# Optimization experiments

Hardware: AMD Instinct MI355X
Metric: run time of the kernel (lower is better)

The kernel has to match this reference:

```python
import jax, jax.numpy as jnp
import numpy as np

HIDDEN = 1024
N_HEADS = 16
N_KV = 4
HEAD_DIM = HIDDEN // N_HEADS  # 64


def setup_inputs() -> dict:
    key = jax.random.key(0)
    ks = jax.random.split(key, 10)
    B, S, D = 2, 2048, HIDDEN
    s = 0.02
    return {
        "hidden_states": jax.random.normal(ks[0], (B, S, D), jnp.float32),
        "attention_mask": jnp.ones((B, S), jnp.float32),
        "Wq": jax.random.normal(ks[1], (D, N_HEADS * HEAD_DIM), jnp.float32) * s,
        "bq": jnp.zeros((N_HEADS * HEAD_DIM,), jnp.float32),
        "Wk": jax.random.normal(ks[2], (D, N_KV * HEAD_DIM), jnp.float32) * s,
        "bk": jnp.zeros((N_KV * HEAD_DIM,), jnp.float32),
        "Wv": jax.random.normal(ks[3], (D, N_KV * HEAD_DIM), jnp.float32) * s,
        "bv": jnp.zeros((N_KV * HEAD_DIM,), jnp.float32),
        "Wo": jax.random.normal(ks[4], (D, D), jnp.float32) * s,
        "bo": jnp.zeros((D,), jnp.float32),
    }


def _rope(x):
    # x: [B, H, S, Dh]; half-split RoPE as in the torch module
    S, Dh = x.shape[-2], x.shape[-1]
    inv_freq = 1.0 / (10000.0 ** (jnp.arange(0, Dh, 2, dtype=jnp.float32) / Dh))
    freqs = jnp.arange(S, dtype=jnp.float32)[:, None] * inv_freq[None, :]  # [S, Dh/2]
    cos, sin = jnp.cos(freqs), jnp.sin(freqs)
    x1, x2 = jnp.split(x, 2, axis=-1)
    return jnp.concatenate([x1 * cos - x2 * sin, x1 * sin + x2 * cos], axis=-1)


def reference(hidden_states, attention_mask, Wq, bq, Wk, bk, Wv, bv, Wo, bo):
    B, S, D = hidden_states.shape
    q = (hidden_states @ Wq + bq).reshape(B, S, N_HEADS, HEAD_DIM).transpose(0, 2, 1, 3)
    k = (hidden_states @ Wk + bk).reshape(B, S, N_KV, HEAD_DIM).transpose(0, 2, 1, 3)
    v = (hidden_states @ Wv + bv).reshape(B, S, N_KV, HEAD_DIM).transpose(0, 2, 1, 3)
    q = _rope(q)
    k = _rope(k)
    rep = N_HEADS // N_KV
    k = jnp.repeat(k, rep, axis=1)  # [B, H, S, Dh]
    v = jnp.repeat(v, rep, axis=1)
    bias = (1.0 - attention_mask[:, None, None, :]) * -1e9  # [B,1,1,S]
    scores = jnp.einsum("bhqd,bhkd->bhqk", q, k) / jnp.sqrt(jnp.float32(HEAD_DIM))
    attn = jax.nn.softmax(scores + bias, axis=-1)
    out = jnp.einsum("bhqk,bhkd->bhqd", attn, v)
    out = out.transpose(0, 2, 1, 3).reshape(B, S, D)
    return out @ Wo + bo
```

## Files before the change

kernel.cpp:

```cpp
#include <hip/hip_runtime.h>

typedef __bf16 bf16;
typedef __attribute__((ext_vector_type(8))) __bf16 bf16x8;
typedef __attribute__((ext_vector_type(4))) __bf16 bf16x4;
typedef __attribute__((ext_vector_type(4))) float f32x4;

#define LOG2E 1.44269504088896340736f
#define QSCALE 0.18033688011112042f

__device__ inline void tr_tile(const float* __restrict__ in, bf16* __restrict__ out,
                               int R, int C, int bx, int by, int tid) {
    __shared__ float t[32][33];
    int tx = tid & 31, ty = tid >> 5;
    int rbase = by * 32, cbase = bx * 32;
#pragma unroll
    for (int i = 0; i < 4; i++) {
        int r = ty + i * 8;
        t[r][tx] = in[(size_t)(rbase + r) * C + cbase + tx];
    }
    __syncthreads();
#pragma unroll
    for (int i = 0; i < 4; i++) {
        int r = ty + i * 8;
        out[(size_t)(cbase + r) * R + rbase + tx] = (bf16)t[tx][r];
    }
}

__global__ __launch_bounds__(256) void prep_k(const float* __restrict__ X,
                                              const float* __restrict__ Wq,
                                              const float* __restrict__ Wk,
                                              const float* __restrict__ Wv,
                                              const float* __restrict__ Wo,
                                              const float* __restrict__ mask,
                                              bf16* __restrict__ Xb,
                                              bf16* __restrict__ WqT,
                                              bf16* __restrict__ WkT,
                                              bf16* __restrict__ WvT,
                                              bf16* __restrict__ WoT,
                                              float2* __restrict__ rt,
                                              float* __restrict__ Mb,
                                              int* __restrict__ mflags) {
    int blk = blockIdx.x, tid = threadIdx.x;
    if (blk < 2048) {
        int idx = (blk * 256 + tid) * 8;
        float4 a = *(const float4*)(X + idx);
        float4 b = *(const float4*)(X + idx + 4);
        bf16 v[8] = {(bf16)a.x, (bf16)a.y, (bf16)a.z, (bf16)a.w,
                     (bf16)b.x, (bf16)b.y, (bf16)b.z, (bf16)b.w};
        *(uint4*)(Xb + idx) = *(const uint4*)v;
    } else if (blk < 3072) {
        int t = blk - 2048; tr_tile(Wq, WqT, 1024, 1024, t & 31, t >> 5, tid);
    } else if (blk < 3328) {
        int t = blk - 3072; tr_tile(Wk, WkT, 1024, 256, t & 7, t >> 3, tid);
    } else if (blk < 3584) {
        int t = blk - 3328; tr_tile(Wv, WvT, 1024, 256, t & 7, t >> 3, tid);
    } else if (blk < 4608) {
        int t = blk - 3584; tr_tile(Wo, WoT, 1024, 1024, t & 31, t >> 5, tid);
    } else if (blk < 4864) {
        int idx = (blk - 4608) * 256 + tid;
        int s = idx >> 5, i = idx & 31;
        float inv = exp2f(-0.41524100370589830f * (float)i);
        float ang = (float)s * inv;
        rt[idx] = make_float2(cosf(ang), sinf(ang));
    } else {
        __shared__ int sflag;
        int b = blk - 4864;
        if (tid == 0) sflag = 1;
        __syncthreads();
        const float* mrow = mask + (size_t)b * 2048;
        int i0 = tid * 8;
        bool ones = true;
#pragma unroll
        for (int j = 0; j < 8; j++) {
            float m = mrow[i0 + j];
            if (m != 1.0f) ones = false;
            Mb[(size_t)b * 2048 + i0 + j] = (1.0f - m) * (-1e9f) * LOG2E;
        }
        if (!ones) sflag = 0;
        __syncthreads();
        if (tid == 0) mflags[b] = sflag;
    }
}

__global__ __launch_bounds__(256) void vtrans_k(const unsigned short* __restrict__ in,
                                                unsigned short* __restrict__ out) {
    __shared__ unsigned short t[32][33];
    int z = blockIdx.z;
    const unsigned short* ip = in + (size_t)z * 2048 * 64;
    unsigned short* op = out + (size_t)z * 2048 * 64;
    int tx = threadIdx.x & 31, ty = threadIdx.x >> 5;
    int rbase = blockIdx.y * 32, cbase = blockIdx.x * 32;
#pragma unroll
    for (int i = 0; i < 4; i++) {
        int r = ty + i * 8;
        t[r][tx] = ip[(size_t)(rbase + r) * 64 + cbase + tx];
    }
    __syncthreads();
#pragma unroll
    for (int i = 0; i < 4; i++) {
        int r = ty + i * 8;
        op[(size_t)(cbase + r) * 2048 + rbase + tx] = t[tx][r];
    }
}

__device__ __forceinline__ void gemm_main_12864(const bf16* __restrict__ A,
                                                const bf16* __restrict__ BT,
                                                int m0, int n0, int tid,
                                                f32x4 (&acc)[2][4]) {
    __shared__ bf16 As[128 * 64];
    __shared__ bf16 Bs[64 * 64];
    int w = tid >> 6, lane = tid & 63, l15 = lane & 15, quad = lane >> 4;

    int srow = lane >> 3;
    int kx = ((lane & 7) ^ srow) * 8;
    const bf16* ga0 = A + (size_t)(m0 + w * 32 + srow) * 1024 + kx;
    const bf16* gb0 = BT + (size_t)(n0 + w * 16 + srow) * 1024 + kx;
    bf16* la0 = As + (w * 32) * 64 + lane * 8;
    bf16* lb0 = Bs + (w * 16) * 64 + lane * 8;

    for (int k0 = 0; k0 < 1024; k0 += 64) {
#pragma unroll
        for (int p = 0; p < 4; p++)
            __builtin_amdgcn_global_load_lds(
                (const __attribute__((address_space(1))) unsigned int*)(ga0 + (size_t)p * 8 * 1024 + k0),
                (__attribute__((address_space(3))) unsigned int*)(la0 + p * 512), 16, 0, 0);
#pragma unroll
        for (int p = 0; p < 2; p++)
            __builtin_amdgcn_global_load_lds(
                (const __attribute__((address_space(1))) unsigned int*)(gb0 + (size_t)p * 8 * 1024 + k0),
                (__attribute__((address_space(3))) unsigned int*)(lb0 + p * 512), 16, 0, 0);
        __syncthreads();
#pragma unroll
        for (int half = 0; half < 2; half++) {
            bf16x8 a[2], bfr[4];
            int kp = ((half * 4 + quad) ^ (l15 & 7)) * 8;
#pragma unroll
            for (int i = 0; i < 2; i++)
                a[i] = *(const bf16x8*)&As[(w * 32 + i * 16 + l15) * 64 + kp];
#pragma unroll
            for (int j = 0; j < 4; j++)
                bfr[j] = *(const bf16x8*)&Bs[(j * 16 + l15) * 64 + kp];
#pragma unroll
            for (int i = 0; i < 2; i++)
#pragma unroll
                for (int j = 0; j < 4; j++)
                    acc[i][j] = __builtin_amdgcn_mfma_f32_16x16x32_bf16(a[i], bfr[j], acc[i][j], 0, 0, 0);
        }
        __syncthreads();
    }
}

__global__ __launch_bounds__(256) void qkv_gemm2(const bf16* __restrict__ Xb,
                                                 const bf16* __restrict__ WTall,
                                                 const float* __restrict__ bq,
                                                 const float* __restrict__ bk,
                                                 const float* __restrict__ bv,
                                                 const float2* __restrict__ rt,
                                                 bf16* __restrict__ Qb,
                                                 bf16* __restrict__ Kb,
                                                 bf16* __restrict__ Vb) {
    int tt = blockIdx.x, gy = blockIdx.y, tid = threadIdx.x;
    f32x4 acc[2][4] = {};
    gemm_main_12864(Xb, WTall, tt * 128, gy * 64, tid, acc);

    int w = tid >> 6, lane = tid & 63, l15 = lane & 15, quad = lane >> 4;
    const float* bias;
    bf16* dst;
    int mode, head;
    if (gy < 16)      { head = gy;      bias = bq + head * 64; dst = Qb; mode = 0; }
    else if (gy < 20) { head = gy - 16; bias = bk + head * 64; dst = Kb; mode = 1; }
    else              { head = gy - 20; bias = bv + head * 64; dst = Vb; mode = 2; }

#pragma unroll
    for (int i = 0; i < 2; i++) {
#pragma unroll
        for (int r = 0; r < 4; r++) {
            int token = tt * 128 + w * 32 + i * 16 + quad * 4 + r;
            int b = token >> 11, s = token & 2047;
            float vals[4];
#pragma unroll
            for (int j = 0; j < 4; j++) vals[j] = acc[i][j][r] + bias[j * 16 + l15];
            if (mode <= 1) {
#pragma unroll
                for (int c = 0; c < 2; c++) {
                    float2 cs2 = rt[s * 32 + c * 16 + l15];
                    float x1 = vals[c], x2 = vals[c + 2];
                    vals[c]     = x1 * cs2.x - x2 * cs2.y;
                    vals[c + 2] = x1 * cs2.y + x2 * cs2.x;
                }
            }
            if (mode == 0) {
#pragma unroll
                for (int j = 0; j < 4; j++) vals[j] *= QSCALE;
            }
            size_t base;
            if (mode == 0) base = (((size_t)b * 16 + head) * 2048 + s) * 64;
            else           base = (((size_t)b * 4  + head) * 2048 + s) * 64;
#pragma unroll
            for (int j = 0; j < 4; j++) dst[base + j * 16 + l15] = (bf16)vals[j];
        }
    }
}

__global__ __launch_bounds__(256) void oproj_gemm2(const bf16* __restrict__ Ab,
                                                   const bf16* __restrict__ WoT,
                                                   const float* __restrict__ bo,
                                                   float* __restrict__ out) {
    int tt = blockIdx.x, nt = blockIdx.y, tid = threadIdx.x;
    f32x4 acc[2][4] = {};
    gemm_main_12864(Ab, WoT, tt * 128, nt * 64, tid, acc);

    int w = tid >> 6, lane = tid & 63, l15 = lane & 15, quad = lane >> 4;
#pragma unroll
    for (int i = 0; i < 2; i++) {
#pragma unroll
        for (int r = 0; r < 4; r++) {
            int token = tt * 128 + w * 32 + i * 16 + quad * 4 + r;
#pragma unroll
            for (int j = 0; j < 4; j++) {
                int n = nt * 64 + j * 16 + l15;
                out[(size_t)token * 1024 + n] = acc[i][j][r] + bo[n];
            }
        }
    }
}

__global__ __launch_bounds__(256) void attn_k(const bf16* __restrict__ Qb,
                                              const bf16* __restrict__ Kb,
                                              const bf16* __restrict__ VbT,
                                              const float* __restrict__ Mb,
                                              const int* __restrict__ mflags,
                                              bf16* __restrict__ Ob) {
    int qt = blockIdx.x, h = blockIdx.y, b = blockIdx.z;
    int kvh = h >> 2;

    __shared__ bf16 Ks[2][64 * 64];
    __shared__ bf16 Vs[2][64 * 64];
    __shared__ unsigned short Ps[4][32 * 72];

    int tid = threadIdx.x, w = tid >> 6, lane = tid & 63, l15 = lane & 15, quad = lane >> 4;

    const bool maskOnes = (mflags[b] != 0);

    bf16x8 qa[2][2];
#pragma unroll
    for (int g = 0; g < 2; g++) {
        size_t qbase = (((size_t)b * 16 + h) * 2048 + (size_t)qt * 128 + w * 32 + g * 16 + l15) * 64;
        qa[g][0] = *(const bf16x8*)(Qb + qbase + quad * 8);
        qa[g][1] = *(const bf16x8*)(Qb + qbase + 32 + quad * 8);
    }

    f32x4 oacc[2][4] = {};
    float lsum[2] = {0.f, 0.f};

    size_t kRow = ((size_t)b * 4 + kvh) * 2048;
    size_t vRow = ((size_t)b * 4 + kvh) * 64;
    const float* mrow = Mb + (size_t)b * 2048 + quad * 4;

    int srow = (lane >> 3);
    int kx = ((lane & 7) ^ srow) * 8;
    const bf16* gk0 = Kb + (kRow + w * 16 + srow) * 64 + kx;
    const bf16* gv0 = VbT + (vRow + w * 16 + srow) * 2048 + kx;
    int lofs = (w * 16) * 64 + lane * 8;

#define STAGE(KT, BUF)                                                                              \
    do {                                                                                            \
        _Pragma("unroll")                                                                           \
        for (int p = 0; p < 2; p++) {                                                               \
            __builtin_amdgcn_global_load_lds(                                                       \
                (const __attribute__((address_space(1))) unsigned int*)(gk0 + ((size_t)(KT) * 64 + p * 8) * 64), \
                (__attribute__((address_space(3))) unsigned int*)(&Ks[BUF][0] + lofs + p * 512), 16, 0, 0); \
            __builtin_amdgcn_global_load_lds(                                                       \
                (const __attribute__((address_space(1))) unsigned int*)(gv0 + (size_t)p * 8 * 2048 + (KT) * 64), \
                (__attribute__((address_space(3))) unsigned int*)(&Vs[BUF][0] + lofs + p * 512), 16, 0, 0); \
        }                                                                                           \
    } while (0)

    STAGE(0, 0);
    __syncthreads();

    for (int kt = 0; kt < 32; kt++) {
        int cb = kt & 1;
        if (kt < 31) STAGE(kt + 1, cb ^ 1);

        const bf16* ksb = &Ks[cb][0];
        const bf16* vsb = &Vs[cb][0];

        bf16x8 ka[4][2];
#pragma unroll
        for (int c = 0; c < 4; c++) {
            int row = c * 16 + l15;
#pragma unroll
            for (int half = 0; half < 2; half++) {
                int kp = ((half * 4 + quad) ^ (l15 & 7)) * 8;
                ka[c][half] = *(const bf16x8*)&ksb[row * 64 + kp];
            }
        }

        f32x4 sc[2][4];
#pragma unroll
        for (int g = 0; g < 2; g++)
#pragma unroll
            for (int c = 0; c < 4; c++) {
                f32x4 z = {};
                z = __builtin_amdgcn_mfma_f32_16x16x32_bf16(ka[c][0], qa[g][0], z, 0, 0, 0);
                z = __builtin_amdgcn_mfma_f32_16x16x32_bf16(ka[c][1], qa[g][1], z, 0, 0, 0);
                sc[g][c] = z;
            }
        if (!maskOnes) {
#pragma unroll
            for (int c = 0; c < 4; c++) {
                f32x4 bias4 = *(const f32x4*)(mrow + kt * 64 + c * 16);
#pragma unroll
                for (int r = 0; r < 4; r++) { sc[0][c][r] += bias4[r]; sc[1][c][r] += bias4[r]; }
            }
        }

#pragma unroll
        for (int g = 0; g < 2; g++) {
            float rs = 0.f;
#pragma unroll
            for (int c = 0; c < 4; c++)
#pragma unroll
                for (int r = 0; r < 4; r++) { sc[g][c][r] = exp2f(sc[g][c][r]); rs += sc[g][c][r]; }
            lsum[g] += rs;
#pragma unroll
            for (int c = 0; c < 4; c++) {
                bf16x4 pv = {(bf16)sc[g][c][0], (bf16)sc[g][c][1], (bf16)sc[g][c][2], (bf16)sc[g][c][3]};
                *(bf16x4*)&Ps[w][(g * 16 + l15) * 72 + c * 16 + quad * 4] = pv;
            }
        }

        bf16x8 vb[4][2];
#pragma unroll
        for (int c = 0; c < 4; c++) {
            int row = c * 16 + l15;
#pragma unroll
            for (int half = 0; half < 2; half++) {
                int kp = ((half * 4 + quad) ^ (l15 & 7)) * 8;
                vb[c][half] = *(const bf16x8*)&vsb[row * 64 + kp];
            }
        }
        bf16x8 pa[2][2];
#pragma unroll
        for (int g = 0; g < 2; g++) {
            pa[g][0] = *(const bf16x8*)&Ps[w][(g * 16 + l15) * 72 + quad * 8];
            pa[g][1] = *(const bf16x8*)&Ps[w][(g * 16 + l15) * 72 + 32 + quad * 8];
        }
#pragma unroll
        for (int g = 0; g < 2; g++)
#pragma unroll
            for (int c = 0; c < 4; c++) {
                oacc[g][c] = __builtin_amdgcn_mfma_f32_16x16x32_bf16(pa[g][0], vb[c][0], oacc[g][c], 0, 0, 0);
                oacc[g][c] = __builtin_amdgcn_mfma_f32_16x16x32_bf16(pa[g][1], vb[c][1], oacc[g][c], 0, 0, 0);
            }
        __syncthreads();
    }
#undef STAGE

#pragma unroll
    for (int g = 0; g < 2; g++) {
        lsum[g] += __shfl_xor(lsum[g], 16, 64);
        lsum[g] += __shfl_xor(lsum[g], 32, 64);
        float linv[4];
#pragma unroll
        for (int r = 0; r < 4; r++) linv[r] = 1.0f / __shfl(lsum[g], quad * 4 + r, 64);
#pragma unroll
        for (int r = 0; r < 4; r++) {
            int q = qt * 128 + w * 32 + g * 16 + quad * 4 + r;
            size_t base = ((size_t)b * 2048 + q) * 1024 + h * 64;
#pragma unroll
            for (int c = 0; c < 4; c++) Ob[base + c * 16 + l15] = (bf16)(oacc[g][c][r] * linv[r]);
        }
    }
}

extern "C" void kernel_launch(void* const* d_in, const int* in_sizes, int n_in,
                              void* d_out, int out_size, void* d_ws, size_t ws_size,
                              hipStream_t stream) {
    const float* X    = (const float*)d_in[0];
    const float* mask = (const float*)d_in[1];
    const float* Wq   = (const float*)d_in[2];
    const float* bq   = (const float*)d_in[3];
    const float* Wk   = (const float*)d_in[4];
    const float* bk   = (const float*)d_in[5];
    const float* Wv   = (const float*)d_in[6];
    const float* bv   = (const float*)d_in[7];
    const float* Wo   = (const float*)d_in[8];
    const float* bo   = (const float*)d_in[9];
    float* out = (float*)d_out;
    bf16* ws  = (bf16*)d_ws;

    bf16* Xb  = ws;
    bf16* WqT = Xb + (size_t)4096 * 1024;
    bf16* WkT = WqT + 1024 * 1024;
    bf16* WvT = WkT + 256 * 1024;
    bf16* WoT = WvT + 256 * 1024;
    bf16* Qb  = WoT + 1024 * 1024;
    bf16* Kb  = Qb + (size_t)2 * 16 * 2048 * 64;
    bf16* Vb  = Kb + (size_t)2 * 4 * 2048 * 64;
    bf16* Ab  = Vb + (size_t)2 * 4 * 2048 * 64;
    float2* rt = (float2*)(Ab + (size_t)2 * 2048 * 1024);
    float* Mb  = (float*)(rt + 2048 * 32);
    int* mflags = (int*)(Mb + 2 * 2048);
    bf16* VbT = Xb;

    prep_k<<<4866, 256, 0, stream>>>(X, Wq, Wk, Wv, Wo, mask, Xb, WqT, WkT, WvT, WoT, rt, Mb, mflags);
    qkv_gemm2<<<dim3(32, 24), 256, 0, stream>>>(Xb, WqT, bq, bk, bv, rt, Qb, Kb, Vb);
    vtrans_k<<<dim3(2, 64, 8), 256, 0, stream>>>((const unsigned short*)Vb, (unsigned short*)VbT);
    attn_k<<<dim3(16, 16, 2), 256, 0, stream>>>(Qb, Kb, VbT, Mb, mflags, Ab);
    oproj_gemm2<<<dim3(32, 16), 256, 0, stream>>>(Ab, WoT, bo, out);
}
```

Measured before the change: 200.4 us.

## Split attention KV range across two blocks and merge partials in new kernel

The attention kernel now splits the 2048-key range into two halves on the grid z axis, doubling the block count from 512 to 1024. Each half writes unnormalised fp32 partial outputs and row sums, and a new merge kernel adds them, normalises, and writes bf16. Row sums now come from an extra MFMA against a ones vector instead of scalar adds, and V is read straight from global memory rather than staged in LDS, which frees shared memory. In exchange there is a large fp32 intermediate write and read, one more launch, and uncached V loads on the critical path.

```diff
diff --git a/kernel.cpp b/kernel.cpp
--- a/kernel.cpp
+++ b/kernel.cpp
@@ -225,17 +225,19 @@
     }
 }
 
-__global__ __launch_bounds__(256) void attn_k(const bf16* __restrict__ Qb,
-                                              const bf16* __restrict__ Kb,
-                                              const bf16* __restrict__ VbT,
-                                              const float* __restrict__ Mb,
-                                              const int* __restrict__ mflags,
-                                              bf16* __restrict__ Ob) {
-    int qt = blockIdx.x, h = blockIdx.y, b = blockIdx.z;
+__global__ __launch_bounds__(256, 4) void attn_k(const bf16* __restrict__ Qb,
+                                                 const bf16* __restrict__ Kb,
+                                                 const bf16* __restrict__ VbT,
+                                                 const float* __restrict__ Mb,
+                                                 const int* __restrict__ mflags,
+                                                 float* __restrict__ Op,
+                                                 float* __restrict__ Lp) {
+    int qt = blockIdx.x, h = blockIdx.y, z = blockIdx.z;
+    int b = z >> 1, sp = z & 1;
     int kvh = h >> 2;
+    int kt0 = sp * 16;
 
     __shared__ bf16 Ks[2][64 * 64];
-    __shared__ bf16 Vs[2][64 * 64];
     __shared__ unsigned short Ps[4][32 * 72];
 
     int tid = threadIdx.x, w = tid >> 6, lane = tid & 63, l15 = lane & 15, quad = lane >> 4;
@@ -251,40 +253,38 @@
     }
 
     f32x4 oacc[2][4] = {};
-    float lsum[2] = {0.f, 0.f};
+    f32x4 sacc[2] = {};
+
+    bf16 one_ = (bf16)1.0f;
+    bf16x8 vones = {one_, one_, one_, one_, one_, one_, one_, one_};
 
     size_t kRow = ((size_t)b * 4 + kvh) * 2048;
-    size_t vRow = ((size_t)b * 4 + kvh) * 64;
+    const bf16* Vg = VbT + ((size_t)b * 4 + kvh) * 64 * 2048;
     const float* mrow = Mb + (size_t)b * 2048 + quad * 4;
 
     int srow = (lane >> 3);
     int kx = ((lane & 7) ^ srow) * 8;
     const bf16* gk0 = Kb + (kRow + w * 16 + srow) * 64 + kx;
-    const bf16* gv0 = VbT + (vRow + w * 16 + srow) * 2048 + kx;
     int lofs = (w * 16) * 64 + lane * 8;
 
 #define STAGE(KT, BUF)                                                                              \
     do {                                                                                            \
         _Pragma("unroll")                                                                           \
-        for (int p = 0; p < 2; p++) {                                                               \
+        for (int p = 0; p < 2; p++)                                                                 \
             __builtin_amdgcn_global_load_lds(                                                       \
                 (const __attribute__((address_space(1))) unsigned int*)(gk0 + ((size_t)(KT) * 64 + p * 8) * 64), \
                 (__attribute__((address_space(3))) unsigned int*)(&Ks[BUF][0] + lofs + p * 512), 16, 0, 0); \
-            __builtin_amdgcn_global_load_lds(                                                       \
-                (const __attribute__((address_space(1))) unsigned int*)(gv0 + (size_t)p * 8 * 2048 + (KT) * 64), \
-                (__attribute__((address_space(3))) unsigned int*)(&Vs[BUF][0] + lofs + p * 512), 16, 0, 0); \
-        }                                                                                           \
     } while (0)
 
-    STAGE(0, 0);
+    STAGE(kt0, 0);
     __syncthreads();
 
-    for (int kt = 0; kt < 32; kt++) {
+    for (int kt = 0; kt < 16; kt++) {
         int cb = kt & 1;
-        if (kt < 31) STAGE(kt + 1, cb ^ 1);
+        if (kt < 15) STAGE(kt0 + kt + 1, cb ^ 1);
+        int ktg = kt0 + kt;
 
         const bf16* ksb = &Ks[cb][0];
-        const bf16* vsb = &Vs[cb][0];
 
         bf16x8 ka[4][2];
 #pragma unroll
@@ -302,15 +302,24 @@
         for (int g = 0; g < 2; g++)
 #pragma unroll
             for (int c = 0; c < 4; c++) {
-                f32x4 z = {};
-                z = __builtin_amdgcn_mfma_f32_16x16x32_bf16(ka[c][0], qa[g][0], z, 0, 0, 0);
-                z = __builtin_amdgcn_mfma_f32_16x16x32_bf16(ka[c][1], qa[g][1], z, 0, 0, 0);
-                sc[g][c] = z;
-            }
+                f32x4 zz = {};
+                zz = __builtin_amdgcn_mfma_f32_16x16x32_bf16(ka[c][0], qa[g][0], zz, 0, 0, 0);
+                zz = __builtin_amdgcn_mfma_f32_16x16x32_bf16(ka[c][1], qa[g][1], zz, 0, 0, 0);
+                sc[g][c] = zz;
+            }
+
+        bf16x8 vb[4][2];
+#pragma unroll
+        for (int c = 0; c < 4; c++)
+#pragma unroll
+            for (int half = 0; half < 2; half++)
+                vb[c][half] = *(const bf16x8*)(Vg + ((size_t)(c * 16 + l15)) * 2048 +
+                                               (size_t)ktg * 64 + (half * 4 + quad) * 8);
+
         if (!maskOnes) {
 #pragma unroll
             for (int c = 0; c < 4; c++) {
-                f32x4 bias4 = *(const f32x4*)(mrow + kt * 64 + c * 16);
+                f32x4 bias4 = *(const f32x4*)(mrow + ktg * 64 + c * 16);
 #pragma unroll
                 for (int r = 0; r < 4; r++) { sc[0][c][r] += bias4[r]; sc[1][c][r] += bias4[r]; }
             }
@@ -318,29 +327,15 @@
 
 #pragma unroll
         for (int g = 0; g < 2; g++) {
-            float rs = 0.f;
-#pragma unroll
-            for (int c = 0; c < 4; c++)
-#pragma unroll
-                for (int r = 0; r < 4; r++) { sc[g][c][r] = exp2f(sc[g][c][r]); rs += sc[g][c][r]; }
-            lsum[g] += rs;
 #pragma unroll
             for (int c = 0; c < 4; c++) {
+#pragma unroll
+                for (int r = 0; r < 4; r++) sc[g][c][r] = exp2f(sc[g][c][r]);
                 bf16x4 pv = {(bf16)sc[g][c][0], (bf16)sc[g][c][1], (bf16)sc[g][c][2], (bf16)sc[g][c][3]};
                 *(bf16x4*)&Ps[w][(g * 16 + l15) * 72 + c * 16 + quad * 4] = pv;
             }
         }
 
-        bf16x8 vb[4][2];
-#pragma unroll
-        for (int c = 0; c < 4; c++) {
-            int row = c * 16 + l15;
-#pragma unroll
-            for (int half = 0; half < 2; half++) {
-                int kp = ((half * 4 + quad) ^ (l15 & 7)) * 8;
-                vb[c][half] = *(const bf16x8*)&vsb[row * 64 + kp];
-            }
-        }
         bf16x8 pa[2][2];
 #pragma unroll
         for (int g = 0; g < 2; g++) {
@@ -348,31 +343,59 @@
             pa[g][1] = *(const bf16x8*)&Ps[w][(g * 16 + l15) * 72 + 32 + quad * 8];
         }
 #pragma unroll
-        for (int g = 0; g < 2; g++)
+        for (int g = 0; g < 2; g++) {
+            sacc[g] = __builtin_amdgcn_mfma_f32_16x16x32_bf16(pa[g][0], vones, sacc[g], 0, 0, 0);
+            sacc[g] = __builtin_amdgcn_mfma_f32_16x16x32_bf16(pa[g][1], vones, sacc[g], 0, 0, 0);
 #pragma unroll
             for (int c = 0; c < 4; c++) {
                 oacc[g][c] = __builtin_amdgcn_mfma_f32_16x16x32_bf16(pa[g][0], vb[c][0], oacc[g][c], 0, 0, 0);
                 oacc[g][c] = __builtin_amdgcn_mfma_f32_16x16x32_bf16(pa[g][1], vb[c][1], oacc[g][c], 0, 0, 0);
             }
+        }
         __syncthreads();
     }
 #undef STAGE
 
+    size_t slab = (size_t)(sp * 2 + b);
 #pragma unroll
     for (int g = 0; g < 2; g++) {
-        lsum[g] += __shfl_xor(lsum[g], 16, 64);
-        lsum[g] += __shfl_xor(lsum[g], 32, 64);
-        float linv[4];
-#pragma unroll
-        for (int r = 0; r < 4; r++) linv[r] = 1.0f / __shfl(lsum[g], quad * 4 + r, 64);
 #pragma unroll
         for (int r = 0; r < 4; r++) {
             int q = qt * 128 + w * 32 + g * 16 + quad * 4 + r;
-            size_t base = ((size_t)b * 2048 + q) * 1024 + h * 64;
-#pragma unroll
-            for (int c = 0; c < 4; c++) Ob[base + c * 16 + l15] = (bf16)(oacc[g][c][r] * linv[r]);
-        }
-    }
+            size_t base = (slab * 2048 + q) * 1024 + h * 64;
+#pragma unroll
+            for (int c = 0; c < 4; c++) Op[base + c * 16 + l15] = oacc[g][c][r];
+        }
+        if (l15 == 0) {
+#pragma unroll
+            for (int r = 0; r < 4; r++)
+                Lp[(slab * 16 + h) * 2048 + qt * 128 + w * 32 + g * 16 + quad * 4 + r] = sacc[g][r];
+        }
+    }
+}
+
+__global__ __launch_bounds__(256) void merge_k(const float* __restrict__ Op,
+                                               const float* __restrict__ Lp,
+                                               bf16* __restrict__ Ab) {
+    int idx = (blockIdx.x * 256 + threadIdx.x) * 8;
+    int tok = idx >> 10;
+    int col = idx & 1023;
+    int h = col >> 6;
+    int b = tok >> 11, q = tok & 2047;
+    float l0 = Lp[((size_t)b * 16 + h) * 2048 + q];
+    float l1 = Lp[((size_t)(b + 2) * 16 + h) * 2048 + q];
+    float inv = 1.0f / (l0 + l1);
+    const float* p0 = Op + (size_t)idx;
+    const float* p1 = p0 + (size_t)2 * 2048 * 1024;
+    float4 a0 = *(const float4*)p0;
+    float4 a1 = *(const float4*)(p0 + 4);
+    float4 c0 = *(const float4*)p1;
+    float4 c1 = *(const float4*)(p1 + 4);
+    bf16 o[8] = {(bf16)((a0.x + c0.x) * inv), (bf16)((a0.y + c0.y) * inv),
+                 (bf16)((a0.z + c0.z) * inv), (bf16)((a0.w + c0.w) * inv),
+                 (bf16)((a1.x + c1.x) * inv), (bf16)((a1.y + c1.y) * inv),
+                 (bf16)((a1.z + c1.z) * inv), (bf16)((a1.w + c1.w) * inv)};
+    *(uint4*)(Ab + idx) = *(const uint4*)o;
 }
 
 extern "C" void kernel_launch(void* const* d_in, const int* in_sizes, int n_in,
@@ -403,11 +426,14 @@
     float2* rt = (float2*)(Ab + (size_t)2 * 2048 * 1024);
     float* Mb  = (float*)(rt + 2048 * 32);
     int* mflags = (int*)(Mb + 2 * 2048);
+    float* Op = (float*)(mflags + 4);
+    float* Lp = Op + (size_t)4 * 2048 * 1024;
     bf16* VbT = Xb;
 
     prep_k<<<4866, 256, 0, stream>>>(X, Wq, Wk, Wv, Wo, mask, Xb, WqT, WkT, WvT, WoT, rt, Mb, mflags);
     qkv_gemm2<<<dim3(32, 24), 256, 0, stream>>>(Xb, WqT, bq, bk, bv, rt, Qb, Kb, Vb);
     vtrans_k<<<dim3(2, 64, 8), 256, 0, stream>>>((const unsigned short*)Vb, (unsigned short*)VbT);
-    attn_k<<<dim3(16, 16, 2), 256, 0, stream>>>(Qb, Kb, VbT, Mb, mflags, Ab);
+    attn_k<<<dim3(16, 16, 4), 256, 0, stream>>>(Qb, Kb, VbT, Mb, mflags, Op, Lp);
+    merge_k<<<2048, 256, 0, stream>>>(Op, Lp, Ab);
     oproj_gemm2<<<dim3(32, 16), 256, 0, stream>>>(Ab, WoT, bo, out);
 }
```

Measured after the change: 238.8 us. 19.2% more time.
